# Performance work log

Hardware: AMD Instinct MI355X
Metric: run time of the kernel (lower is better)

Reference implementation:

```python
import jax, jax.numpy as jnp
import numpy as np

N, E, IN_DIM, OUT_DIM, H = 50000, 800000, 128, 16, 8


def setup_inputs() -> dict:
    key = jax.random.key(0)
    ks = jax.random.split(key, 10)
    h = jax.random.normal(ks[0], (N, IN_DIM), dtype=jnp.float32)
    row = jnp.sort(jax.random.randint(ks[1], (E,), 0, N))
    col = jax.random.randint(ks[2], (E,), 0, N)
    s = 1.0 / np.sqrt(IN_DIM)
    Wq = jax.random.normal(ks[3], (IN_DIM, OUT_DIM * H), dtype=jnp.float32) * s
    Wk = jax.random.normal(ks[4], (IN_DIM, OUT_DIM * H), dtype=jnp.float32) * s
    Wv = jax.random.normal(ks[5], (IN_DIM, OUT_DIM * H), dtype=jnp.float32) * s
    bq = jnp.zeros((OUT_DIM * H,), jnp.float32)
    bk = jnp.zeros((OUT_DIM * H,), jnp.float32)
    bv = jnp.zeros((OUT_DIM * H,), jnp.float32)
    return {"h": h, "Wq": Wq, "bq": bq, "Wk": Wk, "bk": bk, "Wv": Wv, "bv": bv,
            "row": row, "col": col}


def reference(h, Wq, bq, Wk, bk, Wv, bv, row, col):
    n = h.shape[0]
    scaling = OUT_DIM ** (-0.5)
    # projections, reshaped (N, out_dim, heads) as in the torch module
    q = (h @ Wq + bq).reshape(n, OUT_DIM, H) * scaling
    k = (h @ Wk + bk).reshape(n, OUT_DIM, H)
    v = (h @ Wv + bv).reshape(n, OUT_DIM, H)
    # bsddmm: per-edge, per-head dot product  score[e,h] = <q[row[e],:,h], k[col[e],:,h]>
    s = jnp.einsum('edh,edh->eh', q[row], k[col])  # [E, H]
    # sparse row-wise softmax (over each destination node's neighbors)
    m = jax.ops.segment_max(s, row, num_segments=n)       # [N, H]
    p = jnp.exp(s - m[row])                               # [E, H]
    z = jax.ops.segment_sum(p, row, num_segments=n)       # [N, H]
    attn = p / z[row]                                     # [E, H]
    # bspmm: out[i,d,h] = sum_{e: row[e]=i} attn[e,h] * v[col[e],d,h]
    out = jax.ops.segment_sum(attn[:, None, :] * v[col], row, num_segments=n)
    return out.reshape(n, -1)
```

## Files before the change

### kernel.cpp

```cpp
#include <hip/hip_runtime.h>
#include <math.h>

typedef unsigned int uint32;
typedef short short8 __attribute__((ext_vector_type(8)));
typedef float f32x4 __attribute__((ext_vector_type(4)));


__device__ __forceinline__ uint32 pack_bf16(float lo, float hi) {
    uint32 a = __float_as_uint(lo);
    uint32 b = __float_as_uint(hi);
    a = (a + 0x7FFFu + ((a >> 16) & 1u)) >> 16;
    b = (b + 0x7FFFu + ((b >> 16) & 1u)) & 0xFFFF0000u;
    return a | b;
}
__device__ __forceinline__ unsigned short bf16r(float x) {
    uint32 u = __float_as_uint(x);
    return (unsigned short)((u + 0x7FFFu + ((u >> 16) & 1u)) >> 16);
}

__global__ __launch_bounds__(256) void transpose_W_kernel(
    const float* __restrict__ Wq, const float* __restrict__ Wk,
    const float* __restrict__ Wv, unsigned short* __restrict__ Wt)
{
    __shared__ unsigned short tile[128][129];
    const int m = blockIdx.x;
    const float* W = (m == 0) ? Wq : (m == 1) ? Wk : Wv;
    const int t = threadIdx.x;

    const float4* W4 = reinterpret_cast<const float4*>(W);
    #pragma unroll
    for (int i0 = 0; i0 < 16; ++i0) {
        int i = t + i0 * 256;
        int k = i >> 5, nq = i & 31;
        float4 v = W4[i];
        tile[nq * 4 + 0][k] = bf16r(v.x);
        tile[nq * 4 + 1][k] = bf16r(v.y);
        tile[nq * 4 + 2][k] = bf16r(v.z);
        tile[nq * 4 + 3][k] = bf16r(v.w);
    }
    __syncthreads();
    uint32* out = reinterpret_cast<uint32*>(Wt) + (size_t)m * 8192;
    #pragma unroll
    for (int i0 = 0; i0 < 32; ++i0) {
        int i = t + i0 * 256;
        int n = i >> 6, kp = i & 63;
        uint32 lo = tile[n][kp * 2], hi = tile[n][kp * 2 + 1];
        out[i] = lo | (hi << 16);
    }
}

__global__ __launch_bounds__(256) void proj_mfma_kernel(
    const float* __restrict__ h, const unsigned short* __restrict__ Wt,
    const float* __restrict__ bq, const float* __restrict__ bk,
    const float* __restrict__ bv,
    uint32* __restrict__ Qp, uint32* __restrict__ KVp, int N)
{
    __shared__ unsigned char smem[16384 + 32768];
    const int t = threadIdx.x;
    const int nbase = blockIdx.x * 64;
    const int mat = blockIdx.y;

    {
        const float4* h4 = reinterpret_cast<const float4*>(h);
        #pragma unroll
        for (int i0 = 0; i0 < 8; ++i0) {
            int j = t + i0 * 256;
            int row = j >> 5, q = j & 31;
            float4 v = make_float4(0.f, 0.f, 0.f, 0.f);
            if (nbase + row < N) v = h4[(size_t)(nbase + row) * 32 + q];
            int slot = q >> 1, half = q & 1;
            uint2 w = make_uint2(pack_bf16(v.x, v.y), pack_bf16(v.z, v.w));
            int byte = row * 256 + ((slot ^ (row & 7)) << 4) + half * 8;
            *reinterpret_cast<uint2*>(&smem[byte]) = w;
        }
    }
    {
        const uint4* wg = reinterpret_cast<const uint4*>(Wt + (size_t)mat * 16384);
        #pragma unroll
        for (int i0 = 0; i0 < 8; ++i0) {
            int j = t + i0 * 256;
            int row = j >> 4, slot = j & 15;
            uint4 v = wg[j];
            int byte = 16384 + row * 256 + ((slot ^ (row & 7)) << 4);
            *reinterpret_cast<uint4*>(&smem[byte]) = v;
        }
    }
    __syncthreads();

    const int lane = t & 63;
    const int wv = t >> 6;
    const int r = lane & 15, g = lane >> 4;
    const int mbase = wv * 16;

    short8 afr[4];
    #pragma unroll
    for (int kb = 0; kb < 4; ++kb) {
        int row = mbase + r;
        int byte = row * 256 + (((kb * 4 + g) ^ (row & 7)) << 4);
        afr[kb] = *reinterpret_cast<const short8*>(&smem[byte]);
    }

    f32x4 acc[8];
    #pragma unroll
    for (int tt = 0; tt < 8; ++tt) acc[tt] = (f32x4){0.f, 0.f, 0.f, 0.f};

    #pragma unroll
    for (int tt = 0; tt < 8; ++tt) {
        int nrow = tt * 16 + r;
        #pragma unroll
        for (int kb = 0; kb < 4; ++kb) {
            int byte = 16384 + nrow * 256 + (((kb * 4 + g) ^ (nrow & 7)) << 4);
            short8 bfr = *reinterpret_cast<const short8*>(&smem[byte]);
            acc[tt] = __builtin_amdgcn_mfma_f32_16x16x32_bf16(afr[kb], bfr, acc[tt], 0, 0, 0);
        }
    }

    const float* bias = (mat == 0) ? bq : (mat == 1) ? bk : bv;
    const float SCALE_Q = 0.25f * 1.44269504f;
    #pragma unroll
    for (int tt = 0; tt < 4; ++tt) {
        int c = tt * 16 + r;
        float blo = bias[c], bhi = bias[c + 64];
        #pragma unroll
        for (int reg = 0; reg < 4; ++reg) {
            int node = nbase + mbase + g * 4 + reg;
            if (node < N) {
                float lo = acc[tt][reg] + blo;
                float hi = acc[tt + 4][reg] + bhi;
                size_t idx = (size_t)node * 64 + c;
                if (mat == 0) Qp[idx] = pack_bf16(lo * SCALE_Q, hi * SCALE_Q);
                else          KVp[idx * 2 + (mat - 1)] = pack_bf16(lo, hi);
            }
        }
    }
}

__global__ void row_ptr_kernel(const int* __restrict__ row, int* __restrict__ rp,
                               int N, int E)
{
    int i = blockIdx.x * blockDim.x + threadIdx.x;
    if (i > N) return;
    int lo = 0, hi = E;
    while (lo < hi) {
        int mid = (lo + hi) >> 1;
        if (row[mid] < i) lo = mid + 1; else hi = mid;
    }
    rp[i] = lo;
}

__global__ __launch_bounds__(256) void edge_attn_kernel(
    const uint32* __restrict__ Qp, const uint2* __restrict__ KV,
    const int* __restrict__ rp, const int* __restrict__ col,
    float* __restrict__ out, int N)
{
    const int lane = threadIdx.x & 63;
    const int node = blockIdx.x * 4 + (threadIdx.x >> 6);
    if (node >= N) return;

    const int start = rp[node], end = rp[node + 1];
    float* outp = out + (size_t)node * 128;
    if (start >= end) { outp[lane] = 0.f; outp[lane + 64] = 0.f; return; }
    const int last = end - 1;

    const uint32 qu = Qp[(size_t)node * 64 + lane];
    const float q0 = __uint_as_float(qu << 16);
    const float q1 = __uint_as_float(qu & 0xFFFF0000u);

    float z = 0.f, a0 = 0.f, a1 = 0.f;

    uint2 kva[4];
    #pragma unroll
    for (int d = 0; d < 4; ++d) {
        int c = col[min(start + d, last)];
        kva[d] = KV[(size_t)c * 64 + lane];
    }

    for (int g = start; g < end; g += 4) {
        uint2 kvb[4];
        #pragma unroll
        for (int d = 0; d < 4; ++d) {
            int c = col[min(g + 4 + d, last)];
            kvb[d] = KV[(size_t)c * 64 + lane];
        }
        #pragma unroll
        for (int d = 0; d < 4; ++d) {
            if (g + d < end) {
                const float k0 = __uint_as_float(kva[d].x << 16);
                const float k1 = __uint_as_float(kva[d].x & 0xFFFF0000u);
                const float v0 = __uint_as_float(kva[d].y << 16);
                const float v1 = __uint_as_float(kva[d].y & 0xFFFF0000u);
                float s = fmaf(q0, k0, q1 * k1);
                s += __shfl_xor(s, 8);
                s += __shfl_xor(s, 16);
                s += __shfl_xor(s, 32);
                const float p = __builtin_amdgcn_exp2f(s);
                z += p;
                a0 = fmaf(p, v0, a0);
                a1 = fmaf(p, v1, a1);
            }
        }
        #pragma unroll
        for (int d = 0; d < 4; ++d) kva[d] = kvb[d];
    }

    const float rz = 1.0f / z;
    outp[lane]      = a0 * rz;
    outp[lane + 64] = a1 * rz;
}

extern "C" void kernel_launch(void* const* d_in, const int* in_sizes, int n_in,
                              void* d_out, int out_size, void* d_ws, size_t ws_size,
                              hipStream_t stream)
{
    const float* h  = (const float*)d_in[0];
    const float* Wq = (const float*)d_in[1];
    const float* bq = (const float*)d_in[2];
    const float* Wk = (const float*)d_in[3];
    const float* bk = (const float*)d_in[4];
    const float* Wv = (const float*)d_in[5];
    const float* bv = (const float*)d_in[6];
    const int* row  = (const int*)d_in[7];
    const int* col  = (const int*)d_in[8];
    float* out = (float*)d_out;

    const int N = in_sizes[0] / 128;
    const int E = in_sizes[7];

    uint2*  KV = (uint2*)d_ws;
    uint32* Qp = (uint32*)(KV + (size_t)N * 64);
    unsigned short* Wt = (unsigned short*)(Qp + (size_t)N * 64);
    int*    rp = (int*)(Wt + 3 * 16384);

    transpose_W_kernel<<<3, 256, 0, stream>>>(Wq, Wk, Wv, Wt);
    row_ptr_kernel<<<(N + 256) / 256, 256, 0, stream>>>(row, rp, N, E);
    proj_mfma_kernel<<<dim3((N + 63) / 64, 3), 256, 0, stream>>>(
        h, Wt, bq, bk, bv, Qp, (uint32*)KV, N);
    edge_attn_kernel<<<(N + 3) / 4, 256, 0, stream>>>(Qp, KV, rp, col, out, N);
}
```

Baseline: 111.8 us.

## Fuse Q/K/V projections per block and deepen edge gather prefetch

The projection kernel no longer launches one block per matrix. Each block now loads its h rows once directly into MFMA register fragments, with no LDS staging, and computes Q, K and V in sequence, reading weight fragments straight from global memory. K and V results are packed together so each node's KV pair goes out as a single uint2 store instead of two strided 32-bit writes. This removes reading h three times and the LDS staging cost, but it adds uncoalesced global weight loads and more register pressure. Separately, the edge attention loop now prefetches 8 neighbor KV rows per step instead of 4 and pipelines the col index loads a further step ahead, for more memory-level parallelism.

```diff
diff --git a/kernel.cpp b/kernel.cpp
--- a/kernel.cpp
+++ b/kernel.cpp
@@ -4,6 +4,8 @@
 typedef unsigned int uint32;
 typedef short short8 __attribute__((ext_vector_type(8)));
 typedef float f32x4 __attribute__((ext_vector_type(4)));
+
+union frag_u { short8 s; uint32 u[4]; uint4 q; };
 
 
 __device__ __forceinline__ uint32 pack_bf16(float lo, float hi) {
@@ -20,7 +22,7 @@
 
 __global__ __launch_bounds__(256) void transpose_W_kernel(
     const float* __restrict__ Wq, const float* __restrict__ Wk,
-    const float* __restrict__ Wv, unsigned short* __restrict__ Wt)
+    const float* __restrict__ Wv, uint32* __restrict__ Wt)
 {
     __shared__ unsigned short tile[128][129];
     const int m = blockIdx.x;
@@ -39,97 +41,85 @@
         tile[nq * 4 + 3][k] = bf16r(v.w);
     }
     __syncthreads();
-    uint32* out = reinterpret_cast<uint32*>(Wt) + (size_t)m * 8192;
+    uint32* out = Wt + (size_t)m * 8192;
     #pragma unroll
     for (int i0 = 0; i0 < 32; ++i0) {
         int i = t + i0 * 256;
         int n = i >> 6, kp = i & 63;
-        uint32 lo = tile[n][kp * 2], hi = tile[n][kp * 2 + 1];
-        out[i] = lo | (hi << 16);
+        out[i] = (uint32)tile[n][kp * 2] | ((uint32)tile[n][kp * 2 + 1] << 16);
     }
 }
 
 __global__ __launch_bounds__(256) void proj_mfma_kernel(
-    const float* __restrict__ h, const unsigned short* __restrict__ Wt,
+    const float* __restrict__ h, const uint32* __restrict__ Wt,
     const float* __restrict__ bq, const float* __restrict__ bk,
     const float* __restrict__ bv,
-    uint32* __restrict__ Qp, uint32* __restrict__ KVp, int N)
-{
-    __shared__ unsigned char smem[16384 + 32768];
+    uint32* __restrict__ Qp, uint2* __restrict__ KV, int N)
+{
     const int t = threadIdx.x;
-    const int nbase = blockIdx.x * 64;
-    const int mat = blockIdx.y;
-
-    {
-        const float4* h4 = reinterpret_cast<const float4*>(h);
-        #pragma unroll
-        for (int i0 = 0; i0 < 8; ++i0) {
-            int j = t + i0 * 256;
-            int row = j >> 5, q = j & 31;
-            float4 v = make_float4(0.f, 0.f, 0.f, 0.f);
-            if (nbase + row < N) v = h4[(size_t)(nbase + row) * 32 + q];
-            int slot = q >> 1, half = q & 1;
-            uint2 w = make_uint2(pack_bf16(v.x, v.y), pack_bf16(v.z, v.w));
-            int byte = row * 256 + ((slot ^ (row & 7)) << 4) + half * 8;
-            *reinterpret_cast<uint2*>(&smem[byte]) = w;
-        }
-    }
-    {
-        const uint4* wg = reinterpret_cast<const uint4*>(Wt + (size_t)mat * 16384);
-        #pragma unroll
-        for (int i0 = 0; i0 < 8; ++i0) {
-            int j = t + i0 * 256;
-            int row = j >> 4, slot = j & 15;
-            uint4 v = wg[j];
-            int byte = 16384 + row * 256 + ((slot ^ (row & 7)) << 4);
-            *reinterpret_cast<uint4*>(&smem[byte]) = v;
-        }
-    }
-    __syncthreads();
-
     const int lane = t & 63;
     const int wv = t >> 6;
     const int r = lane & 15, g = lane >> 4;
-    const int mbase = wv * 16;
-
-    short8 afr[4];
+    const int nbase = blockIdx.x * 64;
+
+    const int arow = nbase + wv * 16 + r;
+    const bool av = arow < N;
+    const float4* h4 = reinterpret_cast<const float4*>(h);
+    frag_u afr[4];
     #pragma unroll
     for (int kb = 0; kb < 4; ++kb) {
-        int row = mbase + r;
-        int byte = row * 256 + (((kb * 4 + g) ^ (row & 7)) << 4);
-        afr[kb] = *reinterpret_cast<const short8*>(&smem[byte]);
-    }
-
-    f32x4 acc[8];
-    #pragma unroll
-    for (int tt = 0; tt < 8; ++tt) acc[tt] = (f32x4){0.f, 0.f, 0.f, 0.f};
-
-    #pragma unroll
-    for (int tt = 0; tt < 8; ++tt) {
-        int nrow = tt * 16 + r;
-        #pragma unroll
-        for (int kb = 0; kb < 4; ++kb) {
-            int byte = 16384 + nrow * 256 + (((kb * 4 + g) ^ (nrow & 7)) << 4);
-            short8 bfr = *reinterpret_cast<const short8*>(&smem[byte]);
-            acc[tt] = __builtin_amdgcn_mfma_f32_16x16x32_bf16(afr[kb], bfr, acc[tt], 0, 0, 0);
-        }
-    }
-
-    const float* bias = (mat == 0) ? bq : (mat == 1) ? bk : bv;
+        float4 x = make_float4(0.f,0.f,0.f,0.f), y = x;
+        if (av) {
+            size_t base = (size_t)arow * 32 + (kb * 4 + g) * 2;
+            x = h4[base]; y = h4[base + 1];
+        }
+        afr[kb].u[0] = pack_bf16(x.x, x.y);
+        afr[kb].u[1] = pack_bf16(x.z, x.w);
+        afr[kb].u[2] = pack_bf16(y.x, y.y);
+        afr[kb].u[3] = pack_bf16(y.z, y.w);
+    }
+
     const float SCALE_Q = 0.25f * 1.44269504f;
-    #pragma unroll
-    for (int tt = 0; tt < 4; ++tt) {
-        int c = tt * 16 + r;
-        float blo = bias[c], bhi = bias[c + 64];
-        #pragma unroll
-        for (int reg = 0; reg < 4; ++reg) {
-            int node = nbase + mbase + g * 4 + reg;
-            if (node < N) {
+    uint32 kpk[4][4];
+
+    #pragma unroll
+    for (int mat = 0; mat < 3; ++mat) {
+        f32x4 acc[8];
+        #pragma unroll
+        for (int tt = 0; tt < 8; ++tt) acc[tt] = (f32x4){0.f, 0.f, 0.f, 0.f};
+
+        const uint32* wb = Wt + mat * 8192;
+        #pragma unroll
+        for (int tt = 0; tt < 8; ++tt) {
+            #pragma unroll
+            for (int kb = 0; kb < 4; ++kb) {
+                frag_u bfr;
+                bfr.q = *reinterpret_cast<const uint4*>(
+                            wb + (tt * 16 + r) * 64 + (kb * 4 + g) * 4);
+                acc[tt] = __builtin_amdgcn_mfma_f32_16x16x32_bf16(
+                              afr[kb].s, bfr.s, acc[tt], 0, 0, 0);
+            }
+        }
+
+        const float* bias = (mat == 0) ? bq : (mat == 1) ? bk : bv;
+        #pragma unroll
+        for (int tt = 0; tt < 4; ++tt) {
+            int c = tt * 16 + r;
+            float blo = bias[c], bhi = bias[c + 64];
+            #pragma unroll
+            for (int reg = 0; reg < 4; ++reg) {
+                int node = nbase + wv * 16 + g * 4 + reg;
                 float lo = acc[tt][reg] + blo;
                 float hi = acc[tt + 4][reg] + bhi;
-                size_t idx = (size_t)node * 64 + c;
-                if (mat == 0) Qp[idx] = pack_bf16(lo * SCALE_Q, hi * SCALE_Q);
-                else          KVp[idx * 2 + (mat - 1)] = pack_bf16(lo, hi);
+                if (mat == 0) {
+                    if (node < N)
+                        Qp[(size_t)node * 64 + c] = pack_bf16(lo * SCALE_Q, hi * SCALE_Q);
+                } else if (mat == 1) {
+                    kpk[tt][reg] = pack_bf16(lo, hi);
+                } else {
+                    if (node < N)
+                        KV[(size_t)node * 64 + c] = make_uint2(kpk[tt][reg], pack_bf16(lo, hi));
+                }
             }
         }
     }
@@ -168,27 +158,30 @@
 
     float z = 0.f, a0 = 0.f, a1 = 0.f;
 
-    uint2 kva[4];
-    #pragma unroll
-    for (int d = 0; d < 4; ++d) {
-        int c = col[min(start + d, last)];
-        kva[d] = KV[(size_t)c * 64 + lane];
-    }
-
-    for (int g = start; g < end; g += 4) {
-        uint2 kvb[4];
-        #pragma unroll
-        for (int d = 0; d < 4; ++d) {
-            int c = col[min(g + 4 + d, last)];
-            kvb[d] = KV[(size_t)c * 64 + lane];
-        }
-        #pragma unroll
-        for (int d = 0; d < 4; ++d) {
-            if (g + d < end) {
-                const float k0 = __uint_as_float(kva[d].x << 16);
-                const float k1 = __uint_as_float(kva[d].x & 0xFFFF0000u);
-                const float v0 = __uint_as_float(kva[d].y << 16);
-                const float v1 = __uint_as_float(kva[d].y & 0xFFFF0000u);
+    int cb[8];
+    #pragma unroll
+    for (int d = 0; d < 8; ++d) cb[d] = col[min(start + d, last)];
+    uint2 kv[8];
+    #pragma unroll
+    for (int d = 0; d < 8; ++d) kv[d] = KV[(size_t)cb[d] * 64 + lane];
+    #pragma unroll
+    for (int d = 0; d < 8; ++d) cb[d] = col[min(start + 8 + d, last)];
+
+    for (int gb = start; gb < end; gb += 8) {
+        uint2 kvn[8];
+        #pragma unroll
+        for (int d = 0; d < 8; ++d)
+            kvn[d] = KV[(size_t)cb[d] * 64 + lane];
+        #pragma unroll
+        for (int d = 0; d < 8; ++d)
+            cb[d] = col[min(gb + 16 + d, last)];
+        #pragma unroll
+        for (int d = 0; d < 8; ++d) {
+            if (gb + d < end) {
+                const float k0 = __uint_as_float(kv[d].x << 16);
+                const float k1 = __uint_as_float(kv[d].x & 0xFFFF0000u);
+                const float v0 = __uint_as_float(kv[d].y << 16);
+                const float v1 = __uint_as_float(kv[d].y & 0xFFFF0000u);
                 float s = fmaf(q0, k0, q1 * k1);
                 s += __shfl_xor(s, 8);
                 s += __shfl_xor(s, 16);
@@ -200,7 +193,7 @@
             }
         }
         #pragma unroll
-        for (int d = 0; d < 4; ++d) kva[d] = kvb[d];
+        for (int d = 0; d < 8; ++d) kv[d] = kvn[d];
     }
 
     const float rz = 1.0f / z;
@@ -228,12 +221,12 @@
 
     uint2*  KV = (uint2*)d_ws;
     uint32* Qp = (uint32*)(KV + (size_t)N * 64);
-    unsigned short* Wt = (unsigned short*)(Qp + (size_t)N * 64);
-    int*    rp = (int*)(Wt + 3 * 16384);
+    uint32* Wt = Qp + (size_t)N * 64;
+    int*    rp = (int*)(Wt + 3 * 8192);
 
     transpose_W_kernel<<<3, 256, 0, stream>>>(Wq, Wk, Wv, Wt);
     row_ptr_kernel<<<(N + 256) / 256, 256, 0, stream>>>(row, rp, N, E);
-    proj_mfma_kernel<<<dim3((N + 63) / 64, 3), 256, 0, stream>>>(
-        h, Wt, bq, bk, bv, Qp, (uint32*)KV, N);
+    proj_mfma_kernel<<<(N + 63) / 64, 256, 0, stream>>>(
+        h, Wt, bq, bk, bv, Qp, KV, N);
     edge_attn_kernel<<<(N + 3) / 4, 256, 0, stream>>>(Qp, KV, rp, col, out, N);
 }
```

Result: slower. 137.9 us (+23.4%).
